# Performance work log

Measured on AMD Instinct MI355X. Metric: run time of the kernel, lower is better.

## Reference

```python
import jax, jax.numpy as jnp
import numpy as np

EPS = 1e-5

def setup_inputs() -> dict:
    key = jax.random.key(0)
    ks = jax.random.split(key, 4)
    B, C, H, W = 8, 512, 64, 64
    K, V = 64, 512
    x = jax.random.normal(ks[0], (B, C, H, W), dtype=jnp.float32)
    Wq = jax.random.normal(ks[1], (K, C), dtype=jnp.float32) * (1.0 / np.sqrt(C))
    bq = jnp.zeros((K,), dtype=jnp.float32)
    Wk = jax.random.normal(ks[2], (K, C), dtype=jnp.float32) * (1.0 / np.sqrt(C))
    bk = jnp.zeros((K,), dtype=jnp.float32)
    Wv = jax.random.normal(ks[3], (V, C), dtype=jnp.float32) * (1.0 / np.sqrt(C))
    bn_gamma = jnp.ones((V,), dtype=jnp.float32)
    bn_beta = jnp.zeros((V,), dtype=jnp.float32)
    bn_mean = jnp.zeros((V,), dtype=jnp.float32)
    bn_var = jnp.ones((V,), dtype=jnp.float32)
    return {"x": x, "Wq": Wq, "bq": bq, "Wk": Wk, "bk": bk, "Wv": Wv,
            "bn_gamma": bn_gamma, "bn_beta": bn_beta,
            "bn_mean": bn_mean, "bn_var": bn_var}

def reference(x, Wq, bq, Wk, bk, Wv, bn_gamma, bn_beta, bn_mean, bn_var):
    B, C, H, W = x.shape
    N = H * W
    xf = x.reshape(B, C, N)                      # B,C,N
    # 1x1 convs == channel matmuls
    q = jnp.einsum('kc,bcn->bnk', Wq, xf) + bq   # B,N,K  (proj_query permuted)
    k = jnp.einsum('kc,bcn->bkn', Wk, xf) + bk[None, :, None]  # B,K,N
    energy = jnp.einsum('bnk,bkm->bnm', q, k)    # B,N,N
    attention = jax.nn.softmax(energy, axis=-1)  # B,N,N
    # value branch: conv1x1 (no bias) -> BN (inference) -> ReLU
    v = jnp.einsum('vc,bcn->bvn', Wv, xf)        # B,V,N
    scale = bn_gamma / jnp.sqrt(bn_var + EPS)
    shift = bn_beta - bn_mean * scale
    v = jax.nn.relu(v * scale[None, :, None] + shift[None, :, None])
    # out = V @ attention^T
    out = jnp.einsum('bvm,bnm->bvn', v, attention)  # B,V,N
    return out.reshape(B, C, H, W)
```

## Files before the change

### kernel.cpp

```cpp
#include <hip/hip_runtime.h>

typedef __attribute__((ext_vector_type(8))) _Float16 half8;
typedef __attribute__((ext_vector_type(4))) _Float16 half4;
typedef __attribute__((ext_vector_type(4))) float f32x4;

#define BN_EPS 1e-5f
#define LOG2E 1.4426950408889634f

__device__ __forceinline__ void async_copy16(const void* g, void* l) {
  __builtin_amdgcn_global_load_lds((const __attribute__((address_space(1))) void*)g,
                                   (__attribute__((address_space(3))) void*)l,
                                   16, 0, 0);
}

__global__ __launch_bounds__(256) void k_transpose(const float* __restrict__ x,
                                                   _Float16* __restrict__ xT) {
  __shared__ float tile[64][65];
  int n0 = blockIdx.x * 64, c0 = blockIdx.y * 64, b = blockIdx.z;
  const float* xb = x + (size_t)b * 512 * 4096;
  int t = threadIdx.x;
#pragma unroll
  for (int rep = 0; rep < 4; ++rep) {
    int f = rep * 256 + t;
    int c = f >> 4, n4 = f & 15;
    f32x4 v = *(const f32x4*)&xb[(size_t)(c0 + c) * 4096 + n0 + n4 * 4];
    tile[c][n4 * 4 + 0] = v[0];
    tile[c][n4 * 4 + 1] = v[1];
    tile[c][n4 * 4 + 2] = v[2];
    tile[c][n4 * 4 + 3] = v[3];
  }
  __syncthreads();
  _Float16* xTb = xT + (size_t)b * 4096 * 512;
#pragma unroll
  for (int rep = 0; rep < 4; ++rep) {
    int g = rep * 256 + t;
    int n = g >> 4, c4 = g & 15;
    half4 h;
#pragma unroll
    for (int j = 0; j < 4; ++j) h[j] = (_Float16)tile[c4 * 4 + j][n];
    *(half4*)&xTb[(size_t)(n0 + n) * 512 + c0 + c4 * 4] = h;
  }
}

__global__ void k_wall(const float* __restrict__ Wq, const float* __restrict__ Wk,
                       const float* __restrict__ Wv, _Float16* __restrict__ W_all) {
  int i = blockIdx.x * 256 + threadIdx.x;
  if (i >= 640 * 512) return;
  int m = i >> 9, c = i & 511;
  float v;
  if (m < 64) v = Wq[m * 512 + c];
  else if (m < 128) v = Wk[(m - 64) * 512 + c];
  else v = Wv[(m - 128) * 512 + c];
  W_all[i] = (_Float16)v;
}

__global__ __launch_bounds__(256) void k_proj(
    const _Float16* __restrict__ W_all, const _Float16* __restrict__ xT,
    const float* __restrict__ bq, const float* __restrict__ bk,
    const float* __restrict__ gamma, const float* __restrict__ beta,
    const float* __restrict__ mean, const float* __restrict__ var,
    _Float16* __restrict__ q_buf, _Float16* __restrict__ kT_buf,
    _Float16* __restrict__ v_buf) {
  __shared__ __align__(16) _Float16 A_lds[2][128 * 32];
  __shared__ __align__(16) _Float16 B_lds[2][128 * 32];
  int nt = blockIdx.x, mt = blockIdx.y, b = blockIdx.z;
  int t = threadIdx.x, w = t >> 6, lane = t & 63;
  int quad = lane >> 4, l16 = lane & 15;
  int moff = (w & 1) * 64, noff = (w >> 1) * 64;

  f32x4 acc[4][4] = {};

  auto stage = [&](int kk, int buf) {
    int kc = kk * 32;
#pragma unroll
    for (int c = 0; c < 2; ++c) {
      int row = (w * 2 + c) * 16 + (lane >> 2);
      int kseg = (lane & 3) * 8;
      async_copy16(W_all + (size_t)(mt * 128 + row) * 512 + kc + kseg,
                   (char*)A_lds[buf] + (w * 2 + c) * 1024 + lane * 16);
      async_copy16(xT + ((size_t)b * 4096 + nt * 128 + row) * 512 + kc + kseg,
                   (char*)B_lds[buf] + (w * 2 + c) * 1024 + lane * 16);
    }
  };

  stage(0, 0);
  __syncthreads();

#pragma unroll 1
  for (int kk = 0; kk < 16; ++kk) {
    int cur = kk & 1;
    if (kk < 15) stage(kk + 1, cur ^ 1);
    half8 a[4], bb[4];
#pragma unroll
    for (int mi = 0; mi < 4; ++mi)
      a[mi] = *(const half8*)&A_lds[cur][(moff + 16 * mi + l16) * 32 + 8 * quad];
#pragma unroll
    for (int ni = 0; ni < 4; ++ni)
      bb[ni] = *(const half8*)&B_lds[cur][(noff + 16 * ni + l16) * 32 + 8 * quad];
#pragma unroll
    for (int mi = 0; mi < 4; ++mi)
#pragma unroll
      for (int ni = 0; ni < 4; ++ni)
        acc[mi][ni] = __builtin_amdgcn_mfma_f32_16x16x32_f16(a[mi], bb[ni], acc[mi][ni], 0, 0, 0);
    __syncthreads();
  }

  size_t bN = (size_t)b * 4096;
#pragma unroll
  for (int mi = 0; mi < 4; ++mi) {
    int mbase = mt * 128 + moff + 16 * mi + 4 * quad;
#pragma unroll
    for (int ni = 0; ni < 4; ++ni) {
      int n = nt * 128 + noff + 16 * ni + l16;
      if (mbase < 64) {
        half4 h;
#pragma unroll
        for (int i = 0; i < 4; ++i)
          h[i] = (_Float16)((acc[mi][ni][i] + bq[mbase + i]) * LOG2E);
        *(half4*)&q_buf[(bN + n) * 64 + mbase] = h;
      } else if (mbase < 128) {
        half4 h;
#pragma unroll
        for (int i = 0; i < 4; ++i)
          h[i] = (_Float16)(acc[mi][ni][i] + bk[mbase - 64 + i]);
        *(half4*)&kT_buf[(bN + n) * 64 + (mbase - 64)] = h;
      } else {
#pragma unroll
        for (int i = 0; i < 4; ++i) {
          int vv = mbase - 128 + i;
          float sc = gamma[vv] * rsqrtf(var[vv] + BN_EPS);
          float sh = beta[vv] - mean[vv] * sc;
          float r = acc[mi][ni][i] * sc + sh;
          v_buf[((size_t)b * 512 + vv) * 4096 + n] = (_Float16)(r > 0.f ? r : 0.f);
        }
      }
    }
  }
}

__global__ __launch_bounds__(512, 2) void k_flash(
    const _Float16* __restrict__ q_buf, const _Float16* __restrict__ kT_buf,
    const _Float16* __restrict__ v_buf, float* __restrict__ out) {
  __shared__ __align__(16) _Float16 P_lds[2][128 * 72];
  __shared__ __align__(16) _Float16 K_lds[2][64 * 64];
  __shared__ __align__(16) float alpha_lds[2][128];
  __shared__ __align__(8) unsigned char aflag[2][8];
  __shared__ __align__(16) float l_lds[128];
  int bx = blockIdx.x;
  int b = bx & 7;
  int n0 = (bx >> 3) * 128;
  int t = threadIdx.x, w = t >> 6, lane = t & 63, quad = lane >> 4, l16 = lane & 15;
  const _Float16* qb = q_buf + (size_t)b * 4096 * 64;
  const char* kbb = (const char*)(kT_buf + (size_t)b * 4096 * 64);
  const _Float16* vp = v_buf + (size_t)b * 512 * 4096 + (size_t)(64 * w + l16) * 4096 + 8 * quad;

  bool pv_first = (w >= 4);

  int st_r = w * 8 + (lane >> 3);
  int st_c = (lane & 7) ^ (st_r & 7);
  int st_dst = w * 1024 + lane * 16;
  int st_src = st_r * 128 + st_c * 16;

  half8 aq[2];
#pragma unroll
  for (int s = 0; s < 2; ++s)
    aq[s] = *(const half8*)&qb[(size_t)(n0 + 16 * w + l16) * 64 + 32 * s + 8 * quad];

  f32x4 o[8][4] = {};
  float m_st[4], l_st[4];
#pragma unroll
  for (int i = 0; i < 4; ++i) { m_st[i] = -1e30f; l_st[i] = 0.f; }

  auto qk_softmax = [&](const _Float16* Kb, _Float16* Pb, float* Ab,
                        unsigned char* Fb) {
    f32x4 sc[4];
    __builtin_amdgcn_s_setprio(1);
#pragma unroll
    for (int ct = 0; ct < 4; ++ct) {
      int row = 16 * ct + l16;
      int sw = (row & 7) * 16;
      half8 k0 = *(const half8*)((const char*)Kb + row * 128 + ((quad * 16) ^ sw));
      half8 k1 = *(const half8*)((const char*)Kb + row * 128 + (((4 + quad) * 16) ^ sw));
      f32x4 sa = {0.f, 0.f, 0.f, 0.f};
      sa = __builtin_amdgcn_mfma_f32_16x16x32_f16(aq[0], k0, sa, 0, 0, 0);
      sa = __builtin_amdgcn_mfma_f32_16x16x32_f16(aq[1], k1, sa, 0, 0, 0);
      sc[ct] = sa;
    }
    __builtin_amdgcn_s_setprio(0);
    float a_loc[4];
    bool raised = false;
#pragma unroll
    for (int i = 0; i < 4; ++i) {
      float lmax = fmaxf(fmaxf(sc[0][i], sc[1][i]), fmaxf(sc[2][i], sc[3][i]));
      a_loc[i] = 1.f;
      if (__any(lmax > m_st[i] + 8.f)) {
        float mxi = lmax;
#pragma unroll
        for (int off = 1; off < 16; off <<= 1) mxi = fmaxf(mxi, __shfl_xor(mxi, off));
        if (mxi > m_st[i] + 8.f) {
          a_loc[i] = exp2f(m_st[i] - mxi);
          m_st[i] = mxi;
          raised = true;
        }
      }
      float rsum = 0.f;
#pragma unroll
      for (int ct = 0; ct < 4; ++ct) {
        float pv = exp2f(sc[ct][i] - m_st[i]);
        Pb[(16 * w + 4 * quad + i) * 72 + 16 * ct + l16] = (_Float16)pv;
        rsum += pv;
      }
      l_st[i] = l_st[i] * a_loc[i] + rsum;
    }
    bool wr = __any(raised);
    if (wr && l16 == 0) {
#pragma unroll
      for (int i = 0; i < 4; ++i) Ab[16 * w + 4 * quad + i] = a_loc[i];
    }
    if (lane == 0) Fb[w] = wr ? 1 : 0;
  };

  auto rescale = [&](const float* Ab, const unsigned char* Fb) {
    unsigned long long f = *(const unsigned long long*)Fb;
    if (f) {
#pragma unroll
      for (int rt = 0; rt < 8; ++rt) {
        if ((f >> (8 * rt)) & 0xffULL) {
          f32x4 ar = *(const f32x4*)&Ab[16 * rt + 4 * quad];
#pragma unroll
          for (int c2 = 0; c2 < 4; ++c2)
#pragma unroll
            for (int i = 0; i < 4; ++i) o[rt][c2][i] *= ar[i];
        }
      }
    }
  };

  half8 vreg[8];
  auto pv_step = [&](const _Float16* Pb, int mn) {
    __builtin_amdgcn_s_setprio(1);
#pragma unroll
    for (int rt = 0; rt < 8; ++rt) {
      half8 pa0 = *(const half8*)&Pb[(16 * rt + l16) * 72 + 8 * quad];
      half8 pa1 = *(const half8*)&Pb[(16 * rt + l16) * 72 + 32 + 8 * quad];
#pragma unroll
      for (int c2 = 0; c2 < 4; ++c2) {
        o[rt][c2] = __builtin_amdgcn_mfma_f32_16x16x32_f16(pa0, vreg[2 * c2], o[rt][c2], 0, 0, 0);
        o[rt][c2] = __builtin_amdgcn_mfma_f32_16x16x32_f16(pa1, vreg[2 * c2 + 1], o[rt][c2], 0, 0, 0);
      }
    }
    __builtin_amdgcn_s_setprio(0);
#pragma unroll
    for (int c2 = 0; c2 < 4; ++c2) {
      vreg[2 * c2]     = *(const half8*)&vp[c2 * 65536 + mn];
      vreg[2 * c2 + 1] = *(const half8*)&vp[c2 * 65536 + mn + 32];
    }
  };

#pragma unroll
  for (int c2 = 0; c2 < 4; ++c2)
#pragma unroll
    for (int s = 0; s < 2; ++s)
      vreg[2 * c2 + s] = *(const half8*)&vp[c2 * 65536 + 32 * s];
  async_copy16(kbb + st_src, (char*)K_lds[0] + st_dst);
  async_copy16(kbb + 64 * 128 + st_src, (char*)K_lds[1] + st_dst);
  __syncthreads();
  qk_softmax(K_lds[0], P_lds[0], alpha_lds[0], aflag[0]);

#pragma unroll 1
  for (int it = 0; it < 63; ++it) {
    int cur = it & 1, nxt = cur ^ 1;
    __syncthreads();
    int ms = (it + 2 < 64 ? it + 2 : 63) * 64;
    async_copy16(kbb + (size_t)ms * 128 + st_src, (char*)K_lds[cur] + st_dst);
    rescale(alpha_lds[cur], aflag[cur]);
    if (pv_first) {
      pv_step(P_lds[cur], (it + 1) * 64);
      qk_softmax(K_lds[nxt], P_lds[nxt], alpha_lds[nxt], aflag[nxt]);
    } else {
      qk_softmax(K_lds[nxt], P_lds[nxt], alpha_lds[nxt], aflag[nxt]);
      pv_step(P_lds[cur], (it + 1) * 64);
    }
  }
  __syncthreads();
  rescale(alpha_lds[1], aflag[1]);
  pv_step(P_lds[1], 63 * 64);

#pragma unroll
  for (int i = 0; i < 4; ++i) {
    float s = l_st[i];
#pragma unroll
    for (int off = 1; off < 16; off <<= 1) s += __shfl_xor(s, off);
    if (l16 == 0) l_lds[16 * w + 4 * quad + i] = s;
  }
  __syncthreads();
  float* ob = out + (size_t)b * 512 * 4096;
#pragma unroll
  for (int rt = 0; rt < 8; ++rt) {
    f32x4 lv = *(const f32x4*)&l_lds[16 * rt + 4 * quad];
    f32x4 inv;
#pragma unroll
    for (int i = 0; i < 4; ++i) inv[i] = 1.0f / lv[i];
#pragma unroll
    for (int c2 = 0; c2 < 4; ++c2) {
      int vv = 64 * w + 16 * c2 + l16;
      f32x4 res = o[rt][c2] * inv;
      *(f32x4*)(ob + (size_t)vv * 4096 + n0 + 16 * rt + 4 * quad) = res;
    }
  }
}

extern "C" void kernel_launch(void* const* d_in, const int* in_sizes, int n_in,
                              void* d_out, int out_size, void* d_ws, size_t ws_size,
                              hipStream_t stream) {
  const float* x     = (const float*)d_in[0];
  const float* Wq    = (const float*)d_in[1];
  const float* bq    = (const float*)d_in[2];
  const float* Wk    = (const float*)d_in[3];
  const float* bk    = (const float*)d_in[4];
  const float* Wv    = (const float*)d_in[5];
  const float* gamma = (const float*)d_in[6];
  const float* beta  = (const float*)d_in[7];
  const float* mean  = (const float*)d_in[8];
  const float* var   = (const float*)d_in[9];
  float* out = (float*)d_out;

  char* ws = (char*)d_ws;
  _Float16* xT     = (_Float16*)(ws);
  _Float16* W_all  = (_Float16*)(ws + 33554432);
  _Float16* q_buf  = (_Float16*)(ws + 34209792);
  _Float16* kT_buf = (_Float16*)(ws + 38404096);
  _Float16* v_buf  = (_Float16*)(ws + 42598400);

  k_transpose<<<dim3(64, 8, 8), 256, 0, stream>>>(x, xT);
  k_wall<<<dim3(1280), 256, 0, stream>>>(Wq, Wk, Wv, W_all);
  k_proj<<<dim3(32, 5, 8), 256, 0, stream>>>(W_all, xT, bq, bk, gamma, beta, mean, var,
                                             q_buf, kT_buf, v_buf);
  k_flash<<<dim3(256), 512, 0, stream>>>(q_buf, kT_buf, v_buf, out);
}
```

Baseline: 356.2 us.

## Process two key tiles per barrier in flash attention loop

Restructures the flash-attention main loop so each iteration handles a pair of 64-key tiles instead of one. The K, P, alpha and flag LDS buffers are doubled to hold both tiles of a pair, and K tiles are staged two at a time. This halves the number of block-wide barriers and lets more independent work sit between them. The cost is roughly double the shared memory per block, which may stop two 512-thread blocks from fitting on one CU as the launch bounds request.

```diff
diff --git a/kernel.cpp b/kernel.cpp
--- a/kernel.cpp
+++ b/kernel.cpp
@@ -141,10 +141,10 @@
 __global__ __launch_bounds__(512, 2) void k_flash(
     const _Float16* __restrict__ q_buf, const _Float16* __restrict__ kT_buf,
     const _Float16* __restrict__ v_buf, float* __restrict__ out) {
-  __shared__ __align__(16) _Float16 P_lds[2][128 * 72];
-  __shared__ __align__(16) _Float16 K_lds[2][64 * 64];
-  __shared__ __align__(16) float alpha_lds[2][128];
-  __shared__ __align__(8) unsigned char aflag[2][8];
+  __shared__ __align__(16) _Float16 P_lds[2][2][128 * 72];
+  __shared__ __align__(16) _Float16 K_lds[2][2][64 * 64];
+  __shared__ __align__(16) float alpha_lds[2][2][128];
+  __shared__ __align__(8) unsigned char aflag[2][2][8];
   __shared__ __align__(16) float l_lds[128];
   int bx = blockIdx.x;
   int b = bx & 7;
@@ -170,6 +170,11 @@
   float m_st[4], l_st[4];
 #pragma unroll
   for (int i = 0; i < 4; ++i) { m_st[i] = -1e30f; l_st[i] = 0.f; }
+
+  auto stage_pair = [&](int pp, int buf) {
+    async_copy16(kbb + (size_t)(2 * pp) * 8192 + st_src, (char*)K_lds[buf][0] + st_dst);
+    async_copy16(kbb + (size_t)(2 * pp + 1) * 8192 + st_src, (char*)K_lds[buf][1] + st_dst);
+  };
 
   auto qk_softmax = [&](const _Float16* Kb, _Float16* Pb, float* Ab,
                         unsigned char* Fb) {
@@ -262,29 +267,39 @@
 #pragma unroll
     for (int s = 0; s < 2; ++s)
       vreg[2 * c2 + s] = *(const half8*)&vp[c2 * 65536 + 32 * s];
-  async_copy16(kbb + st_src, (char*)K_lds[0] + st_dst);
-  async_copy16(kbb + 64 * 128 + st_src, (char*)K_lds[1] + st_dst);
-  __syncthreads();
-  qk_softmax(K_lds[0], P_lds[0], alpha_lds[0], aflag[0]);
+  stage_pair(0, 0);
+  stage_pair(1, 1);
+  __syncthreads();
+  qk_softmax(K_lds[0][0], P_lds[0][0], alpha_lds[0][0], aflag[0][0]);
+  qk_softmax(K_lds[0][1], P_lds[0][1], alpha_lds[0][1], aflag[0][1]);
 
 #pragma unroll 1
-  for (int it = 0; it < 63; ++it) {
-    int cur = it & 1, nxt = cur ^ 1;
+  for (int p = 0; p < 31; ++p) {
+    int cur = p & 1, nxt = cur ^ 1;
     __syncthreads();
-    int ms = (it + 2 < 64 ? it + 2 : 63) * 64;
-    async_copy16(kbb + (size_t)ms * 128 + st_src, (char*)K_lds[cur] + st_dst);
-    rescale(alpha_lds[cur], aflag[cur]);
+    int pp = (p + 2 < 32) ? p + 2 : 31;
+    stage_pair(pp, cur);
     if (pv_first) {
-      pv_step(P_lds[cur], (it + 1) * 64);
-      qk_softmax(K_lds[nxt], P_lds[nxt], alpha_lds[nxt], aflag[nxt]);
+      rescale(alpha_lds[cur][0], aflag[cur][0]);
+      pv_step(P_lds[cur][0], (2 * p + 1) * 64);
+      qk_softmax(K_lds[nxt][0], P_lds[nxt][0], alpha_lds[nxt][0], aflag[nxt][0]);
+      rescale(alpha_lds[cur][1], aflag[cur][1]);
+      pv_step(P_lds[cur][1], (2 * p + 2) * 64);
+      qk_softmax(K_lds[nxt][1], P_lds[nxt][1], alpha_lds[nxt][1], aflag[nxt][1]);
     } else {
-      qk_softmax(K_lds[nxt], P_lds[nxt], alpha_lds[nxt], aflag[nxt]);
-      pv_step(P_lds[cur], (it + 1) * 64);
-    }
-  }
-  __syncthreads();
-  rescale(alpha_lds[1], aflag[1]);
-  pv_step(P_lds[1], 63 * 64);
+      qk_softmax(K_lds[nxt][0], P_lds[nxt][0], alpha_lds[nxt][0], aflag[nxt][0]);
+      rescale(alpha_lds[cur][0], aflag[cur][0]);
+      pv_step(P_lds[cur][0], (2 * p + 1) * 64);
+      qk_softmax(K_lds[nxt][1], P_lds[nxt][1], alpha_lds[nxt][1], aflag[nxt][1]);
+      rescale(alpha_lds[cur][1], aflag[cur][1]);
+      pv_step(P_lds[cur][1], (2 * p + 2) * 64);
+    }
+  }
+  __syncthreads();
+  rescale(alpha_lds[1][0], aflag[1][0]);
+  pv_step(P_lds[1][0], 63 * 64);
+  rescale(alpha_lds[1][1], aflag[1][1]);
+  pv_step(P_lds[1][1], 63 * 64);
 
 #pragma unroll
   for (int i = 0; i < 4; ++i) {
```

After: 371.1 us. 1.04x slower.
